# Performance work log

Measured on AMD Instinct MI355X. Metric: run time of the kernel, lower is better.

## Reference

```python
import jax, jax.numpy as jnp
import numpy as np

SHAPE_ = 32          # sqrt(max_seq_len); seq positions form a SHAPE_ x SHAPE_ grid
N_HEADS = 8
BATCH = 8
SEQ_LEN = SHAPE_ * SHAPE_  # 1024
HEAD_DIM = 64


def _construct_bias(w_, s):
    """bias[..., j, i] = w_rolled[..., s - i - 1 + j]  -> (1, h, s, s).
    'full' base type: roll last axis left by one (concat of w[...,1:] and w[...,0])."""
    w_ = jnp.concatenate([w_[..., 1:], w_[..., :1]], axis=-1)  # (1, h, 2s-1)
    j = jnp.arange(s)
    i = jnp.arange(s)
    idx = (s - 1 - i)[None, :] + j[:, None]  # (s_j, s_i), values in [0, 2s-2]
    return w_[..., idx]  # (1, h, s, s), axes (..., j, i)


def setup_inputs() -> dict:
    key = jax.random.key(0)
    k1, k2 = jax.random.split(key)
    v = jax.random.normal(k1, (BATCH, SEQ_LEN, N_HEADS, HEAD_DIM), dtype=jnp.float32)
    # learned 1D bias base, length 2*SHAPE_-1 for 'full' base type
    w = jax.random.normal(k2, (1, N_HEADS, 2 * SHAPE_ - 1), dtype=jnp.float32)
    return {"v": v, "w": w}


def reference(v, w):
    s = SHAPE_
    b, L, h, d = v.shape
    bias = _construct_bias(w, s)  # (1, h, s, s)
    # x_ = bias[:, :, None, :, None, :], y_ = bias[:, :, :, None, :, None]
    # w2[., h, a, b, c, e] = bias[., h, b, e] + bias[., h, a, c]  -> (1, h, s, s, s, s)
    w2 = bias[:, :, None, :, None, :] + bias[:, :, :, None, :, None]
    w2 = w2.reshape(1, h, s * s, s * s)  # (1, h, L, L)
    # original: repeat w2 over batch then einsum('nlhd,nhlj->njhd', v, transpose(w2, [0,1,3,2]))
    # => pbv[n, j, h, d] = sum_l v[n, l, h, d] * w2[0, h, j, l]; broadcast instead of repeat.
    return jnp.einsum('nlhd,hjl->njhd', v, w2[0])
```

## Files before the change

### kernel.cpp

```cpp
#include <hip/hip_runtime.h>


#define S 32
#define HD4 128

__global__ __launch_bounds__(128) void reduce_kernel(
    const float4* __restrict__ v, float4* __restrict__ Vc,
    float4* __restrict__ Ve) {
  int block = blockIdx.x;
  int t = threadIdx.x;
  bool isVc = block < 256;
  int b2 = isVc ? block : block - 256;
  int n = b2 >> 5;
  int x = b2 & 31;
  const float4* base = v + (size_t)n * 1024 * HD4 + t;
  float4 acc = make_float4(0.f, 0.f, 0.f, 0.f);
  if (isVc) {
#pragma unroll
    for (int c = 0; c < 32; ++c) {
      float4 r = base[(size_t)(c * S + x) * HD4];
      acc.x += r.x; acc.y += r.y; acc.z += r.z; acc.w += r.w;
    }
    Vc[(size_t)b2 * HD4 + t] = acc;
  } else {
#pragma unroll
    for (int e = 0; e < 32; ++e) {
      float4 r = base[(size_t)(x * S + e) * HD4];
      acc.x += r.x; acc.y += r.y; acc.z += r.z; acc.w += r.w;
    }
    Ve[(size_t)b2 * HD4 + t] = acc;
  }
}

__global__ __launch_bounds__(256) void fused_kernel(
    const float* __restrict__ w,
    const float* __restrict__ Vc, const float* __restrict__ Ve,
    float4* __restrict__ out) {
  __shared__ float bias_s[32][32];
  __shared__ float vc_s[32][64];
  __shared__ float ve_s[32][64];
  __shared__ float t1_s[32][68];
  __shared__ float t2_s[2][68];

  int blk = blockIdx.x;
  int a0 = (blk & 15) << 1;
  int nh = blk >> 4;
  int n = nh >> 3, h = nh & 7;
  int t = threadIdx.x;

  for (int idx = t; idx < 1024; idx += 256) {
    int b = idx >> 5, e = idx & 31;
    bias_s[b][e] = w[h * 63 + (32 + b - e) % 63];
  }
  for (int idx = t; idx < 512; idx += 256) {
    int e = idx >> 4, d4 = idx & 15;
    size_t g = ((size_t)(n * S + e) * 8 + h) * 16 + d4;
    float4 A = ((const float4*)Vc)[g];
    float4 B = ((const float4*)Ve)[g];
    *(float4*)(&vc_s[e][d4 * 4]) = A;
    *(float4*)(&ve_s[e][d4 * 4]) = B;
  }
  __syncthreads();

  int d = t & 63;
  int bg = t >> 6;
  for (int b = bg; b < 32; b += 4) {
    float acc = 0.f;
#pragma unroll
    for (int e = 0; e < 32; ++e) acc += bias_s[b][e] * vc_s[e][d];
    t1_s[b][d] = acc;
  }
  if (bg < 2) {
    float acc = 0.f;
#pragma unroll
    for (int c = 0; c < 32; ++c) acc += bias_s[a0 + bg][c] * ve_s[c][d];
    t2_s[bg][d] = acc;
  }
  __syncthreads();

#pragma unroll
  for (int ar = 0; ar < 2; ++ar) {
    int a = a0 + ar;
#pragma unroll
    for (int it = 0; it < 2; ++it) {
      int idx = it * 256 + t;
      int b = idx >> 4, d4 = idx & 15;
      float4 x = *(const float4*)(&t1_s[b][d4 * 4]);
      float4 y = *(const float4*)(&t2_s[ar][d4 * 4]);
      out[((size_t)(n * 1024 + a * S + b) * 8 + h) * 16 + d4] =
          make_float4(x.x + y.x, x.y + y.y, x.z + y.z, x.w + y.w);
    }
  }
}

extern "C" void kernel_launch(void* const* d_in, const int* in_sizes, int n_in,
                              void* d_out, int out_size, void* d_ws, size_t ws_size,
                              hipStream_t stream) {
  const float* v = (const float*)d_in[0];
  const float* w = (const float*)d_in[1];
  float* out = (float*)d_out;
  float* ws  = (float*)d_ws;

  float* Vc = ws;
  float* Ve = ws + 131072;

  reduce_kernel<<<512, 128, 0, stream>>>((const float4*)v, (float4*)Vc,
                                         (float4*)Ve);
  fused_kernel<<<1024, 256, 0, stream>>>(w, Vc, Ve, (float4*)out);
}
```

Before: 77.58 us.

## Widen fused kernel blocks to cover 8 rows and keep Vc/Ve in registers

The fused kernel now uses 512-thread blocks, each handling 8 output rows instead of 2, with 256 blocks instead of 1024. This cuts the redundant per-block recomputation of the t1 (bias·Vc) product fourfold. Vc/Ve columns are loaded straight into registers, and bias values are read from w with wave-uniform indices instead of building a shared bias table. This removes shared-memory staging and one barrier, at the cost of more registers per thread (64 floats) and fewer blocks to spread across CUs.

Result: slower. 81.53 us (+5.1%).

```diff
diff --git a/kernel.cpp b/kernel.cpp
--- a/kernel.cpp
+++ b/kernel.cpp
@@ -32,64 +32,67 @@
   }
 }
 
-__global__ __launch_bounds__(256) void fused_kernel(
+__global__ __launch_bounds__(512) void fused_kernel(
     const float* __restrict__ w,
     const float* __restrict__ Vc, const float* __restrict__ Ve,
     float4* __restrict__ out) {
-  __shared__ float bias_s[32][32];
-  __shared__ float vc_s[32][64];
-  __shared__ float ve_s[32][64];
-  __shared__ float t1_s[32][68];
-  __shared__ float t2_s[2][68];
+  __shared__ float t1_s[32][64];
+  __shared__ float t2_s[8][64];
 
   int blk = blockIdx.x;
-  int a0 = (blk & 15) << 1;
-  int nh = blk >> 4;
+  int aq = blk & 3;
+  int nh = blk >> 2;
   int n = nh >> 3, h = nh & 7;
   int t = threadIdx.x;
+  int d = t & 63;
+  int bg = __builtin_amdgcn_readfirstlane(t >> 6);
 
-  for (int idx = t; idx < 1024; idx += 256) {
-    int b = idx >> 5, e = idx & 31;
-    bias_s[b][e] = w[h * 63 + (32 + b - e) % 63];
+  const float* wrow = w + h * 63;
+  const float* vcb = Vc + ((size_t)(n * S) * 8 + h) * 64 + d;
+  const float* veb = Ve + ((size_t)(n * S) * 8 + h) * 64 + d;
+
+  float vc[32], ve[32];
+#pragma unroll
+  for (int e = 0; e < 32; ++e) {
+    vc[e] = vcb[(size_t)e * 512];
+    ve[e] = veb[(size_t)e * 512];
   }
-  for (int idx = t; idx < 512; idx += 256) {
-    int e = idx >> 4, d4 = idx & 15;
-    size_t g = ((size_t)(n * S + e) * 8 + h) * 16 + d4;
-    float4 A = ((const float4*)Vc)[g];
-    float4 B = ((const float4*)Ve)[g];
-    *(float4*)(&vc_s[e][d4 * 4]) = A;
-    *(float4*)(&ve_s[e][d4 * 4]) = B;
-  }
-  __syncthreads();
 
-  int d = t & 63;
-  int bg = t >> 6;
-  for (int b = bg; b < 32; b += 4) {
+#pragma unroll
+  for (int kb = 0; kb < 4; ++kb) {
+    int b = kb * 8 + bg;
     float acc = 0.f;
 #pragma unroll
-    for (int e = 0; e < 32; ++e) acc += bias_s[b][e] * vc_s[e][d];
+    for (int e = 0; e < 32; ++e) {
+      int k = 32 + b - e;
+      if (k >= 63) k -= 63;
+      acc += wrow[k] * vc[e];
+    }
     t1_s[b][d] = acc;
   }
-  if (bg < 2) {
+  {
+    int a = aq * 8 + bg;
     float acc = 0.f;
 #pragma unroll
-    for (int c = 0; c < 32; ++c) acc += bias_s[a0 + bg][c] * ve_s[c][d];
+    for (int c = 0; c < 32; ++c) {
+      int k = 32 + a - c;
+      if (k >= 63) k -= 63;
+      acc += wrow[k] * ve[c];
+    }
     t2_s[bg][d] = acc;
   }
   __syncthreads();
 
 #pragma unroll
-  for (int ar = 0; ar < 2; ++ar) {
-    int a = a0 + ar;
-#pragma unroll
-    for (int it = 0; it < 2; ++it) {
-      int idx = it * 256 + t;
-      int b = idx >> 4, d4 = idx & 15;
-      float4 x = *(const float4*)(&t1_s[b][d4 * 4]);
-      float4 y = *(const float4*)(&t2_s[ar][d4 * 4]);
-      out[((size_t)(n * 1024 + a * S + b) * 8 + h) * 16 + d4] =
-          make_float4(x.x + y.x, x.y + y.y, x.z + y.z, x.w + y.w);
-    }
+  for (int i = 0; i < 8; ++i) {
+    int idx = i * 512 + t;
+    int d4 = idx & 15;
+    int brow = (idx >> 4) & 31;
+    int al = idx >> 9;
+    float4 x = *(const float4*)(&t1_s[brow][d4 * 4]);
+    float4 y = *(const float4*)(&t2_s[al][d4 * 4]);
+    out[((size_t)(n * 1024 + (aq * 8 + al) * S + brow) * 8 + h) * 16 + d4] =
+        make_float4(x.x + y.x, x.y + y.y, x.z + y.z, x.w + y.w);
   }
 }
 
@@ -106,5 +109,5 @@
 
   reduce_kernel<<<512, 128, 0, stream>>>((const float4*)v, (float4*)Vc,
                                          (float4*)Ve);
-  fused_kernel<<<1024, 256, 0, stream>>>(w, Vc, Ve, (float4*)out);
+  fused_kernel<<<256, 512, 0, stream>>>(w, Vc, Ve, (float4*)out);
 }
```

## Fuse reduction and bias contraction into one kernel per (n,h,d-slice)

Applied to the files above, without the earlier changes.

Replaces the two-kernel pipeline (global reduce to workspace, then bias contraction) with a single kernel. Each block loads a full 1024x8 slice of v for one batch, head and 8-wide d chunk into shared memory, computes the row and column sums, applies both bias matvecs, and writes the full output slice. This removes the workspace round trip and one launch, but each block now uses about 32KB of LDS and issues narrow strided 32-byte global accesses for both loads and stores.

After: 72.12 us. -7.0%, faster.

```diff
diff --git a/kernel.cpp b/kernel.cpp
--- a/kernel.cpp
+++ b/kernel.cpp
@@ -2,94 +2,81 @@
 
 
 #define S 32
-#define HD4 128
 
-__global__ __launch_bounds__(128) void reduce_kernel(
-    const float4* __restrict__ v, float4* __restrict__ Vc,
-    float4* __restrict__ Ve) {
-  int block = blockIdx.x;
-  int t = threadIdx.x;
-  bool isVc = block < 256;
-  int b2 = isVc ? block : block - 256;
-  int n = b2 >> 5;
-  int x = b2 & 31;
-  const float4* base = v + (size_t)n * 1024 * HD4 + t;
-  float4 acc = make_float4(0.f, 0.f, 0.f, 0.f);
-  if (isVc) {
-#pragma unroll
-    for (int c = 0; c < 32; ++c) {
-      float4 r = base[(size_t)(c * S + x) * HD4];
-      acc.x += r.x; acc.y += r.y; acc.z += r.z; acc.w += r.w;
-    }
-    Vc[(size_t)b2 * HD4 + t] = acc;
-  } else {
-#pragma unroll
-    for (int e = 0; e < 32; ++e) {
-      float4 r = base[(size_t)(x * S + e) * HD4];
-      acc.x += r.x; acc.y += r.y; acc.z += r.z; acc.w += r.w;
-    }
-    Ve[(size_t)b2 * HD4 + t] = acc;
-  }
-}
-
-__global__ __launch_bounds__(256) void fused_kernel(
-    const float* __restrict__ w,
-    const float* __restrict__ Vc, const float* __restrict__ Ve,
-    float4* __restrict__ out) {
-  __shared__ float bias_s[32][32];
-  __shared__ float vc_s[32][64];
-  __shared__ float ve_s[32][64];
-  __shared__ float t1_s[32][68];
-  __shared__ float t2_s[2][68];
+__global__ __launch_bounds__(256) void fused_all(
+    const float4* __restrict__ v4, const float* __restrict__ w,
+    float4* __restrict__ out4) {
+  __shared__ float vs_s[1024][8];
+  __shared__ float bias_s[32][33];
+  __shared__ float vc_s[32][8];
+  __shared__ float ve_s[32][8];
+  __shared__ float t1_s[32][8];
+  __shared__ float t2_s[32][8];
 
   int blk = blockIdx.x;
-  int a0 = (blk & 15) << 1;
-  int nh = blk >> 4;
+  int dq = blk >> 6;
+  int nh = blk & 63;
   int n = nh >> 3, h = nh & 7;
   int t = threadIdx.x;
 
-  for (int idx = t; idx < 1024; idx += 256) {
+#pragma unroll
+  for (int i = 0; i < 4; ++i) {
+    int idx = i * 256 + t;
     int b = idx >> 5, e = idx & 31;
     bias_s[b][e] = w[h * 63 + (32 + b - e) % 63];
   }
-  for (int idx = t; idx < 512; idx += 256) {
-    int e = idx >> 4, d4 = idx & 15;
-    size_t g = ((size_t)(n * S + e) * 8 + h) * 16 + d4;
-    float4 A = ((const float4*)Vc)[g];
-    float4 B = ((const float4*)Ve)[g];
-    *(float4*)(&vc_s[e][d4 * 4]) = A;
-    *(float4*)(&ve_s[e][d4 * 4]) = B;
+
+  const float4* vbase = v4 + ((size_t)(n * 1024) * 8 + h) * 16 + dq * 2;
+#pragma unroll
+  for (int i = 0; i < 8; ++i) {
+    int idx = i * 256 + t;
+    int l = idx >> 1, k = idx & 1;
+    *(float4*)(&vs_s[l][k * 4]) = vbase[(size_t)l * 128 + k];
   }
   __syncthreads();
 
-  int d = t & 63;
-  int bg = t >> 6;
-  for (int b = bg; b < 32; b += 4) {
-    float acc = 0.f;
+  {
+    int x = t >> 3, d = t & 7;
+    float accc = 0.f, acce = 0.f;
 #pragma unroll
-    for (int e = 0; e < 32; ++e) acc += bias_s[b][e] * vc_s[e][d];
-    t1_s[b][d] = acc;
-  }
-  if (bg < 2) {
-    float acc = 0.f;
+    for (int c = 0; c < 32; ++c)
+      accc += vs_s[c * S + x][d];
 #pragma unroll
-    for (int c = 0; c < 32; ++c) acc += bias_s[a0 + bg][c] * ve_s[c][d];
-    t2_s[bg][d] = acc;
+    for (int e = 0; e < 32; ++e) {
+      int e2 = (e + x) & 31;
+      acce += vs_s[x * S + e2][d];
+    }
+    vc_s[x][d] = accc;
+    ve_s[x][d] = acce;
   }
   __syncthreads();
 
+  {
+    int b = t >> 3, d = t & 7;
+    float a1 = 0.f, a2 = 0.f;
 #pragma unroll
-  for (int ar = 0; ar < 2; ++ar) {
-    int a = a0 + ar;
+    for (int e = 0; e < 32; ++e) {
+      int e2 = (e + b) & 31;
+      float bw = bias_s[b][e2];
+      a1 += bw * vc_s[e2][d];
+      a2 += bw * ve_s[e2][d];
+    }
+    t1_s[b][d] = a1;
+    t2_s[b][d] = a2;
+  }
+  __syncthreads();
+
+  float4* obase = out4 + ((size_t)(n * 1024) * 8 + h) * 16 + dq * 2;
 #pragma unroll
-    for (int it = 0; it < 2; ++it) {
-      int idx = it * 256 + t;
-      int b = idx >> 4, d4 = idx & 15;
-      float4 x = *(const float4*)(&t1_s[b][d4 * 4]);
-      float4 y = *(const float4*)(&t2_s[ar][d4 * 4]);
-      out[((size_t)(n * 1024 + a * S + b) * 8 + h) * 16 + d4] =
-          make_float4(x.x + y.x, x.y + y.y, x.z + y.z, x.w + y.w);
-    }
+  for (int i = 0; i < 8; ++i) {
+    int idx = i * 256 + t;
+    int k = idx & 1;
+    int j = idx >> 1;
+    int b = j & 31, a = j >> 5;
+    float4 x = *(const float4*)(&t1_s[b][k * 4]);
+    float4 y = *(const float4*)(&t2_s[a][k * 4]);
+    obase[(size_t)j * 128 + k] =
+        make_float4(x.x + y.x, x.y + y.y, x.z + y.z, x.w + y.w);
   }
 }
 
@@ -99,12 +86,7 @@
   const float* v = (const float*)d_in[0];
   const float* w = (const float*)d_in[1];
   float* out = (float*)d_out;
-  float* ws  = (float*)d_ws;
+  (void)d_ws; (void)ws_size;
 
-  float* Vc = ws;
-  float* Ve = ws + 131072;
-
-  reduce_kernel<<<512, 128, 0, stream>>>((const float4*)v, (float4*)Vc,
-                                         (float4*)Ve);
-  fused_kernel<<<1024, 256, 0, stream>>>(w, Vc, Ve, (float4*)out);
+  fused_all<<<512, 256, 0, stream>>>((const float4*)v, w, (float4*)out);
 }
```
